# Kernel optimization log

Measured on AMD Instinct MI355X. Metric: run time of the kernel, lower is better.

The kernel has to match this reference:

```python
import jax, jax.numpy as jnp
import numpy as np

N = 100000   # nodes
E = 640000   # edges
DIN = 128
DOUT = 128
BN_EPS = 1e-5


def setup_inputs() -> dict:
    key = jax.random.key(0)
    k = jax.random.split(key, 6)
    x = jax.random.normal(k[0], (N, DIN), dtype=jnp.float32)
    edge_index = jax.random.randint(k[1], (2, E), 0, N, dtype=jnp.int64)
    # MLP params: Linear(DIN,DOUT) -> BatchNorm1d(DOUT) -> ReLU -> Linear(DOUT,DOUT)
    s1 = 1.0 / np.sqrt(DIN)
    s2 = 1.0 / np.sqrt(DOUT)
    W1 = jax.random.uniform(k[2], (DIN, DOUT), jnp.float32, -s1, s1)
    b1 = jax.random.uniform(k[3], (DOUT,), jnp.float32, -s1, s1)
    gamma = jnp.ones((DOUT,), jnp.float32)
    beta = jnp.zeros((DOUT,), jnp.float32)
    W2 = jax.random.uniform(k[4], (DOUT, DOUT), jnp.float32, -s2, s2)
    b2 = jax.random.uniform(k[5], (DOUT,), jnp.float32, -s2, s2)
    eps = jnp.zeros((), jnp.float32)  # train_eps=True, init 0.0
    return {"x": x, "edge_index": edge_index, "W1": W1, "b1": b1,
            "gamma": gamma, "beta": beta, "W2": W2, "b2": b2, "eps": eps}


def reference(x, edge_index, W1, b1, gamma, beta, W2, b2, eps):
    src = edge_index[0]
    dst = edge_index[1]
    # GIN sum aggregation: gather source features, scatter-add to target nodes
    agg = jax.ops.segment_sum(x[src], dst, num_segments=N)  # [N, DIN]
    h = agg + (1.0 + eps) * x  # eps-weighted residual combine
    # MLP: Linear -> BatchNorm1d (training stats, biased var) -> ReLU -> Linear
    h = h @ W1 + b1  # [N, DOUT]
    mu = jnp.mean(h, axis=0)
    var = jnp.mean((h - mu) ** 2, axis=0)
    h = (h - mu) * jax.lax.rsqrt(var + BN_EPS) * gamma + beta
    h = jnp.maximum(h, 0.0)
    return h @ W2 + b2
```

## Files before the change

### kernel.cpp

```cpp
#include <hip/hip_runtime.h>

#define N_NODES 100000
#define DIM     128
#define NEDGE   640000
#define BN_EPS  1e-5f
#define NB_SCAN 98

#define PB_X    6250
#define PB_W    64
#define PB_CNT  2500

#define NBUCKET 64
#define T_TILES 4
#define GGRID   1563

typedef __bf16 bf16x8 __attribute__((ext_vector_type(8)));
typedef float  f32x4  __attribute__((ext_vector_type(4)));
typedef unsigned short u16x8 __attribute__((ext_vector_type(8)));

__device__ __forceinline__ unsigned short f2b(float f) {
    unsigned u = __builtin_bit_cast(unsigned, f);
    u += 0x7fffu + ((u >> 16) & 1u);
    return (unsigned short)(u >> 16);
}
__device__ __forceinline__ float b2f(unsigned short b) {
    return __builtin_bit_cast(float, ((unsigned)b) << 16);
}

__global__ __launch_bounds__(256) void k_prep(const float* __restrict__ x,
                                              const float* __restrict__ W1,
                                              const float* __restrict__ W2,
                                              const int* __restrict__ ei,
                                              unsigned short* __restrict__ xb,
                                              unsigned short* __restrict__ Wt1,
                                              unsigned short* __restrict__ Wt2,
                                              int* __restrict__ rowptr,
                                              unsigned short* __restrict__ rank) {
    const int b = blockIdx.x;
    const int t = threadIdx.x;
    if (b < PB_X) {
        size_t base = ((size_t)b * 256 + t) * 8;
        float4 v0 = *(const float4*)(x + base);
        float4 v1 = *(const float4*)(x + base + 4);
        u16x8 o;
        o[0] = f2b(v0.x); o[1] = f2b(v0.y); o[2] = f2b(v0.z); o[3] = f2b(v0.w);
        o[4] = f2b(v1.x); o[5] = f2b(v1.y); o[6] = f2b(v1.z); o[7] = f2b(v1.w);
        *(u16x8*)(xb + base) = o;
    } else if (b < PB_X + PB_W) {
        int idx = (b - PB_X) * 256 + t;
        int k = idx >> 7, n = idx & 127;
        Wt1[n * 128 + k] = f2b(W1[idx]);
    } else if (b < PB_X + 2 * PB_W) {
        int idx = (b - PB_X - PB_W) * 256 + t;
        int k = idx >> 7, n = idx & 127;
        Wt2[n * 128 + k] = f2b(W2[idx]);
    } else {
        int e = (b - PB_X - 2 * PB_W) * 256 + t;
        if (e < NEDGE) {
            int r = atomicAdd(&rowptr[ei[NEDGE + e]], 1);
            rank[e] = (unsigned short)r;
        }
    }
}

__global__ __launch_bounds__(256) void k_scan1(int* __restrict__ rowptr,
                                               int* __restrict__ bsum) {
    __shared__ int tsum[256];
    const int t = threadIdx.x;
    const int base = blockIdx.x * 1024 + t * 4;
    int v[4];
    #pragma unroll
    for (int j = 0; j < 4; ++j)
        v[j] = (base + j < N_NODES) ? rowptr[base + j] : 0;
    int s = v[0] + v[1] + v[2] + v[3];
    tsum[t] = s;
    __syncthreads();
    #pragma unroll
    for (int off = 1; off < 256; off <<= 1) {
        int a = tsum[t];
        int b = (t >= off) ? tsum[t - off] : 0;
        __syncthreads();
        tsum[t] = a + b;
        __syncthreads();
    }
    int run = tsum[t] - s;
    #pragma unroll
    for (int j = 0; j < 4; ++j) {
        int nv = run;
        run += v[j];
        if (base + j < N_NODES) rowptr[base + j] = nv;
    }
    if (t == 255) bsum[blockIdx.x] = tsum[255];
}

__global__ __launch_bounds__(256) void k_scan_add(int* __restrict__ rowptr,
                                                  const int* __restrict__ bsum) {
    __shared__ int sh[128];
    const int t = threadIdx.x;
    if (t < 128) sh[t] = (t < NB_SCAN) ? bsum[t] : 0;
    __syncthreads();
    #pragma unroll
    for (int off = 1; off < 128; off <<= 1) {
        int a = 0, b = 0;
        if (t < 128) { a = sh[t]; b = (t >= off) ? sh[t - off] : 0; }
        __syncthreads();
        if (t < 128) sh[t] = a + b;
        __syncthreads();
    }
    const int add = (blockIdx.x > 0) ? sh[blockIdx.x - 1] : 0;
    const int base = blockIdx.x * 1024 + t * 4;
    #pragma unroll
    for (int j = 0; j < 4; ++j) {
        if (base + j < N_NODES) rowptr[base + j] += add;
    }
    if (blockIdx.x == 0 && t == 0) rowptr[N_NODES] = NEDGE;
}

__global__ __launch_bounds__(256) void k_fill(const int* __restrict__ ei,
                                              const int* __restrict__ rowptr,
                                              const unsigned short* __restrict__ rank,
                                              int* __restrict__ srcidx) {
    int e = blockIdx.x * 256 + threadIdx.x;
    if (e < NEDGE) {
        int dst = ei[NEDGE + e];
        srcidx[rowptr[dst] + (int)rank[e]] = ei[e];
    }
}

__global__ __launch_bounds__(256) void k_agg1(const unsigned short* __restrict__ xb,
                                              const int* __restrict__ rowptr,
                                              const int* __restrict__ srcidx,
                                              const float* __restrict__ epsp,
                                              const unsigned short* __restrict__ Wt,
                                              const float* __restrict__ b1,
                                              unsigned short* __restrict__ hB,
                                              float* __restrict__ buckets) {
    __shared__ float sl[256];
    __shared__ __align__(16) unsigned short At[2][16 * 136];
    __shared__ __align__(16) unsigned short stage[4][512];
    const int t = threadIdx.x;
    const int w = t >> 6;
    const int lane = t & 63;
    const int n15 = lane & 15;
    const int quad = lane >> 4;
    const int c8 = n15 * 8;

    int4 Bfr[2][4];
    const unsigned short* wp = Wt + (w * 32 + n15) * 128 + quad * 8;
    #pragma unroll
    for (int c = 0; c < 2; ++c)
        #pragma unroll
        for (int ks = 0; ks < 4; ++ks)
            Bfr[c][ks] = *(const int4*)(wp + c * 16 * 128 + ks * 32);
    float bias[2] = { b1[w * 32 + n15], b1[w * 32 + 16 + n15] };
    const float scale = 1.0f + epsp[0];

    const int tile0 = blockIdx.x * T_TILES;
    float s[2] = {0.f, 0.f}, q[2] = {0.f, 0.f};
    unsigned short* st = stage[w];

    #pragma unroll
    for (int i = 0; i < T_TILES; ++i) {
        const int row0 = (tile0 + i) * 16;
        const bool valid = row0 < N_NODES;
        unsigned short* al = At[i & 1];
        if (valid) {
            const int node = row0 + w * 4 + quad;
            float acc[8];
            {
                u16x8 v = *(const u16x8*)(xb + (size_t)node * 128 + c8);
                #pragma unroll
                for (int j = 0; j < 8; ++j) acc[j] = scale * b2f(v[j]);
            }
            const int beg = rowptr[node];
            const int end = rowptr[node + 1];
            for (int p = beg; p < end; p += 2) {
                int s0 = srcidx[p];
                u16x8 v0 = *(const u16x8*)(xb + (size_t)s0 * 128 + c8);
                const bool h1 = (p + 1) < end;
                u16x8 v1;
                if (h1) {
                    int s1 = srcidx[p + 1];
                    v1 = *(const u16x8*)(xb + (size_t)s1 * 128 + c8);
                }
                #pragma unroll
                for (int j = 0; j < 8; ++j) acc[j] += b2f(v0[j]);
                if (h1) {
                    #pragma unroll
                    for (int j = 0; j < 8; ++j) acc[j] += b2f(v1[j]);
                }
            }
            u16x8 o;
            #pragma unroll
            for (int j = 0; j < 8; ++j) o[j] = f2b(acc[j]);
            *(u16x8*)(al + (w * 4 + quad) * 136 + c8) = o;
        }
        __syncthreads();
        if (valid) {
            f32x4 accm[2] = {};
            #pragma unroll
            for (int ks = 0; ks < 4; ++ks) {
                int4 araw = *(const int4*)(al + n15 * 136 + ks * 32 + quad * 8);
                bf16x8 af = __builtin_bit_cast(bf16x8, araw);
                #pragma unroll
                for (int c = 0; c < 2; ++c)
                    accm[c] = __builtin_amdgcn_mfma_f32_16x16x32_bf16(
                        af, __builtin_bit_cast(bf16x8, Bfr[c][ks]), accm[c], 0, 0, 0);
            }
            #pragma unroll
            for (int c = 0; c < 2; ++c)
                #pragma unroll
                for (int r = 0; r < 4; ++r) {
                    float v = accm[c][r] + bias[c];
                    s[c] += v; q[c] += v * v;
                    st[(quad * 4 + r) * 32 + c * 16 + n15] = f2b(v);
                }
            int so = lane * 8;
            int r = so >> 5, cc = so & 31;
            *(int4*)(hB + (size_t)(row0 + r) * 128 + w * 32 + cc) = *(const int4*)(st + so);
        }
    }

    #pragma unroll
    for (int c = 0; c < 2; ++c) {
        s[c] += __shfl_down(s[c], 32); q[c] += __shfl_down(q[c], 32);
        s[c] += __shfl_down(s[c], 16); q[c] += __shfl_down(q[c], 16);
    }
    if (quad == 0) {
        #pragma unroll
        for (int c = 0; c < 2; ++c) {
            sl[w * 32 + c * 16 + n15] = s[c];
            sl[128 + w * 32 + c * 16 + n15] = q[c];
        }
    }
    __syncthreads();
    atomicAdd(&buckets[(blockIdx.x & (NBUCKET - 1)) * 256 + t], sl[t]);
}

__global__ void k_finalize(const float* __restrict__ gamma,
                           const float* __restrict__ beta,
                           const float* __restrict__ buckets,
                           float* __restrict__ aff) {
    int c = threadIdx.x;
    if (c < DIM) {
        float s = 0.f, q = 0.f;
        #pragma unroll 8
        for (int b = 0; b < NBUCKET; ++b) {
            s += buckets[b * 256 + c];
            q += buckets[b * 256 + 128 + c];
        }
        float mu  = s * (1.0f / N_NODES);
        float var = q * (1.0f / N_NODES) - mu * mu;
        float a = gamma[c] * rsqrtf(var + BN_EPS);
        aff[c] = a;
        aff[DIM + c] = beta[c] - mu * a;
    }
}

__global__ __launch_bounds__(256) void k_gemm2(const unsigned short* __restrict__ hb,
                                               const unsigned short* __restrict__ Wt2,
                                               const float* __restrict__ aff,
                                               const float* __restrict__ b2,
                                               float* __restrict__ out) {
    __shared__ __align__(16) unsigned short Asb[2][16 * 136];
    __shared__ __align__(16) float stage[4][512];
    const int t = threadIdx.x;
    const int w = t >> 6;
    const int lane = t & 63;
    const int n15 = lane & 15;
    const int quad = lane >> 4;
    const int kb = w * 32 + quad * 8;

    int4 Bfr[2][4];
    const unsigned short* wp = Wt2 + (w * 32 + n15) * 128 + quad * 8;
    #pragma unroll
    for (int c = 0; c < 2; ++c)
        #pragma unroll
        for (int ks = 0; ks < 4; ++ks)
            Bfr[c][ks] = *(const int4*)(wp + c * 16 * 128 + ks * 32);

    float akr[8], bkr[8];
    *(float4*)(akr)     = *(const float4*)(aff + kb);
    *(float4*)(akr + 4) = *(const float4*)(aff + kb + 4);
    *(float4*)(bkr)     = *(const float4*)(aff + 128 + kb);
    *(float4*)(bkr + 4) = *(const float4*)(aff + 128 + kb + 4);
    float bias[2] = { b2[w * 32 + n15], b2[w * 32 + 16 + n15] };

    const int tile0 = blockIdx.x * T_TILES;
    int4 gr;
    {
        int r0 = tile0 * 16;
        if (r0 < N_NODES)
            gr = *(const int4*)(hb + (size_t)(r0 + n15) * 128 + kb);
    }
    float* st = stage[w];

    #pragma unroll
    for (int i = 0; i < T_TILES; ++i) {
        const int row0 = (tile0 + i) * 16;
        const bool valid = row0 < N_NODES;
        unsigned short* al = Asb[i & 1];
        if (valid) {
            u16x8 ar = __builtin_bit_cast(u16x8, gr);
            u16x8 pr;
            #pragma unroll
            for (int j = 0; j < 8; ++j)
                pr[j] = f2b(fmaxf(fmaf(b2f(ar[j]), akr[j], bkr[j]), 0.f));
            *(int4*)(al + n15 * 136 + kb) = __builtin_bit_cast(int4, pr);
        }
        if (i + 1 < T_TILES) {
            int rn = (tile0 + i + 1) * 16;
            if (rn < N_NODES)
                gr = *(const int4*)(hb + (size_t)(rn + n15) * 128 + kb);
        }
        __syncthreads();
        if (valid) {
            f32x4 acc[2] = {};
            #pragma unroll
            for (int ks = 0; ks < 4; ++ks) {
                int4 araw = *(const int4*)(al + n15 * 136 + ks * 32 + quad * 8);
                bf16x8 af = __builtin_bit_cast(bf16x8, araw);
                #pragma unroll
                for (int c = 0; c < 2; ++c)
                    acc[c] = __builtin_amdgcn_mfma_f32_16x16x32_bf16(
                        af, __builtin_bit_cast(bf16x8, Bfr[c][ks]), acc[c], 0, 0, 0);
            }
            #pragma unroll
            for (int c = 0; c < 2; ++c)
                #pragma unroll
                for (int r = 0; r < 4; ++r)
                    st[(quad * 4 + r) * 32 + c * 16 + n15] = acc[c][r] + bias[c];
            #pragma unroll
            for (int p = 0; p < 2; ++p) {
                int fo = p * 256 + lane * 4;
                int r = fo >> 5, cc = fo & 31;
                *(float4*)(out + (size_t)(row0 + r) * 128 + w * 32 + cc) =
                    *(const float4*)(st + fo);
            }
        }
    }
}

extern "C" void kernel_launch(void* const* d_in, const int* in_sizes, int n_in,
                              void* d_out, int out_size, void* d_ws, size_t ws_size,
                              hipStream_t stream) {
    const float* x     = (const float*)d_in[0];
    const int*   ei    = (const int*)d_in[1];
    const float* W1    = (const float*)d_in[2];
    const float* b1    = (const float*)d_in[3];
    const float* gamma = (const float*)d_in[4];
    const float* beta  = (const float*)d_in[5];
    const float* W2    = (const float*)d_in[6];
    const float* b2    = (const float*)d_in[7];
    const float* eps   = (const float*)d_in[8];
    float* out = (float*)d_out;

    float* buckets      = (float*)d_ws;
    int* rowptr         = (int*)(buckets + NBUCKET * 256);
    float* aff          = (float*)(rowptr + N_NODES + 4);
    unsigned short* hB  = (unsigned short*)(aff + 256);
    unsigned short* xb  = hB + (size_t)N_NODES * DIM;
    unsigned short* Wt1 = xb + (size_t)N_NODES * DIM;
    unsigned short* Wt2 = Wt1 + 16384;
    int* srcidx         = (int*)(Wt2 + 16384);
    int* bsum           = srcidx + NEDGE;
    unsigned short* rank = hB;

    hipMemsetAsync(buckets, 0,
                   NBUCKET * 256 * sizeof(float) + (N_NODES + 4) * sizeof(int), stream);

    k_prep<<<PB_X + 2 * PB_W + PB_CNT, 256, 0, stream>>>(x, W1, W2, ei, xb, Wt1, Wt2,
                                                         rowptr, rank);
    k_scan1<<<NB_SCAN, 256, 0, stream>>>(rowptr, bsum);
    k_scan_add<<<NB_SCAN, 256, 0, stream>>>(rowptr, bsum);
    k_fill<<<(NEDGE + 255) / 256, 256, 0, stream>>>(ei, rowptr, rank, srcidx);
    k_agg1<<<GGRID, 256, 0, stream>>>(xb, rowptr, srcidx, eps, Wt1, b1, hB, buckets);
    k_finalize<<<1, 128, 0, stream>>>(gamma, beta, buckets, aff);
    k_gemm2<<<GGRID, 256, 0, stream>>>(hB, Wt2, aff, b2, out);
}
```

Baseline: 240.9 us.

## Process one 16-node tile per aggregation block with 4-way unrolled neighbor gather

The aggregation+GEMM1 kernel now handles a single 16-row tile per block (6250 blocks instead of 1563 blocks looping over 4 tiles). The neighbor gather issues four independent row loads per iteration instead of two. The per-block BN statistics go straight to global atomics from quad-0 lanes, which drops the shared reduction and its barrier. The prep kernel also moves the edge-counting atomics to the first blocks so they start earlier. The aim is more memory-level parallelism and less in-block serialization, at the cost of reloading the W1 fragments in 4x as many blocks and issuing more atomics to the buckets.

After: 229.8 us. -4.6%, faster.

```diff
diff --git a/kernel.cpp b/kernel.cpp
--- a/kernel.cpp
+++ b/kernel.cpp
@@ -6,13 +6,14 @@
 #define BN_EPS  1e-5f
 #define NB_SCAN 98
 
+#define PB_CNT  2500
 #define PB_X    6250
 #define PB_W    64
-#define PB_CNT  2500
 
 #define NBUCKET 64
 #define T_TILES 4
 #define GGRID   1563
+#define AGRID   6250
 
 typedef __bf16 bf16x8 __attribute__((ext_vector_type(8)));
 typedef float  f32x4  __attribute__((ext_vector_type(4)));
@@ -38,28 +39,26 @@
                                               unsigned short* __restrict__ rank) {
     const int b = blockIdx.x;
     const int t = threadIdx.x;
-    if (b < PB_X) {
-        size_t base = ((size_t)b * 256 + t) * 8;
+    if (b < PB_CNT) {
+        int e = b * 256 + t;
+        int r = atomicAdd(&rowptr[ei[NEDGE + e]], 1);
+        rank[e] = (unsigned short)r;
+    } else if (b < PB_CNT + PB_X) {
+        size_t base = ((size_t)(b - PB_CNT) * 256 + t) * 8;
         float4 v0 = *(const float4*)(x + base);
         float4 v1 = *(const float4*)(x + base + 4);
         u16x8 o;
         o[0] = f2b(v0.x); o[1] = f2b(v0.y); o[2] = f2b(v0.z); o[3] = f2b(v0.w);
         o[4] = f2b(v1.x); o[5] = f2b(v1.y); o[6] = f2b(v1.z); o[7] = f2b(v1.w);
         *(u16x8*)(xb + base) = o;
-    } else if (b < PB_X + PB_W) {
-        int idx = (b - PB_X) * 256 + t;
+    } else if (b < PB_CNT + PB_X + PB_W) {
+        int idx = (b - PB_CNT - PB_X) * 256 + t;
         int k = idx >> 7, n = idx & 127;
         Wt1[n * 128 + k] = f2b(W1[idx]);
-    } else if (b < PB_X + 2 * PB_W) {
-        int idx = (b - PB_X - PB_W) * 256 + t;
+    } else {
+        int idx = (b - PB_CNT - PB_X - PB_W) * 256 + t;
         int k = idx >> 7, n = idx & 127;
         Wt2[n * 128 + k] = f2b(W2[idx]);
-    } else {
-        int e = (b - PB_X - 2 * PB_W) * 256 + t;
-        if (e < NEDGE) {
-            int r = atomicAdd(&rowptr[ei[NEDGE + e]], 1);
-            rank[e] = (unsigned short)r;
-        }
     }
 }
 
@@ -135,8 +134,7 @@
                                               const float* __restrict__ b1,
                                               unsigned short* __restrict__ hB,
                                               float* __restrict__ buckets) {
-    __shared__ float sl[256];
-    __shared__ __align__(16) unsigned short At[2][16 * 136];
+    __shared__ __align__(16) unsigned short At[16 * 136];
     __shared__ __align__(16) unsigned short stage[4][512];
     const int t = threadIdx.x;
     const int w = t >> 6;
@@ -145,6 +143,9 @@
     const int quad = lane >> 4;
     const int c8 = n15 * 8;
 
+    const int row0 = blockIdx.x * 16;
+    const int node = row0 + w * 4 + quad;
+
     int4 Bfr[2][4];
     const unsigned short* wp = Wt + (w * 32 + n15) * 128 + quad * 8;
     #pragma unroll
@@ -155,70 +156,71 @@
     float bias[2] = { b1[w * 32 + n15], b1[w * 32 + 16 + n15] };
     const float scale = 1.0f + epsp[0];
 
-    const int tile0 = blockIdx.x * T_TILES;
+    const int beg = rowptr[node];
+    const int end = rowptr[node + 1];
+    float acc[8];
+    {
+        u16x8 v = *(const u16x8*)(xb + (size_t)node * 128 + c8);
+        #pragma unroll
+        for (int j = 0; j < 8; ++j) acc[j] = scale * b2f(v[j]);
+    }
+    for (int p = beg; p < end; p += 4) {
+        const int np = end - p;
+        int i0 = srcidx[p];
+        int i1 = (np > 1) ? srcidx[p + 1] : i0;
+        int i2 = (np > 2) ? srcidx[p + 2] : i0;
+        int i3 = (np > 3) ? srcidx[p + 3] : i0;
+        u16x8 v0 = *(const u16x8*)(xb + (size_t)i0 * 128 + c8);
+        u16x8 v1 = *(const u16x8*)(xb + (size_t)i1 * 128 + c8);
+        u16x8 v2 = *(const u16x8*)(xb + (size_t)i2 * 128 + c8);
+        u16x8 v3 = *(const u16x8*)(xb + (size_t)i3 * 128 + c8);
+        #pragma unroll
+        for (int j = 0; j < 8; ++j) acc[j] += b2f(v0[j]);
+        if (np > 1) {
+            #pragma unroll
+            for (int j = 0; j < 8; ++j) acc[j] += b2f(v1[j]);
+        }
+        if (np > 2) {
+            #pragma unroll
+            for (int j = 0; j < 8; ++j) acc[j] += b2f(v2[j]);
+        }
+        if (np > 3) {
+            #pragma unroll
+            for (int j = 0; j < 8; ++j) acc[j] += b2f(v3[j]);
+        }
+    }
+    {
+        u16x8 o;
+        #pragma unroll
+        for (int j = 0; j < 8; ++j) o[j] = f2b(acc[j]);
+        *(u16x8*)(At + (w * 4 + quad) * 136 + c8) = o;
+    }
+    __syncthreads();
+
+    f32x4 accm[2] = {};
+    #pragma unroll
+    for (int ks = 0; ks < 4; ++ks) {
+        int4 araw = *(const int4*)(At + n15 * 136 + ks * 32 + quad * 8);
+        bf16x8 af = __builtin_bit_cast(bf16x8, araw);
+        #pragma unroll
+        for (int c = 0; c < 2; ++c)
+            accm[c] = __builtin_amdgcn_mfma_f32_16x16x32_bf16(
+                af, __builtin_bit_cast(bf16x8, Bfr[c][ks]), accm[c], 0, 0, 0);
+    }
     float s[2] = {0.f, 0.f}, q[2] = {0.f, 0.f};
     unsigned short* st = stage[w];
-
-    #pragma unroll
-    for (int i = 0; i < T_TILES; ++i) {
-        const int row0 = (tile0 + i) * 16;
-        const bool valid = row0 < N_NODES;
-        unsigned short* al = At[i & 1];
-        if (valid) {
-            const int node = row0 + w * 4 + quad;
-            float acc[8];
-            {
-                u16x8 v = *(const u16x8*)(xb + (size_t)node * 128 + c8);
-                #pragma unroll
-                for (int j = 0; j < 8; ++j) acc[j] = scale * b2f(v[j]);
-            }
-            const int beg = rowptr[node];
-            const int end = rowptr[node + 1];
-            for (int p = beg; p < end; p += 2) {
-                int s0 = srcidx[p];
-                u16x8 v0 = *(const u16x8*)(xb + (size_t)s0 * 128 + c8);
-                const bool h1 = (p + 1) < end;
-                u16x8 v1;
-                if (h1) {
-                    int s1 = srcidx[p + 1];
-                    v1 = *(const u16x8*)(xb + (size_t)s1 * 128 + c8);
-                }
-                #pragma unroll
-                for (int j = 0; j < 8; ++j) acc[j] += b2f(v0[j]);
-                if (h1) {
-                    #pragma unroll
-                    for (int j = 0; j < 8; ++j) acc[j] += b2f(v1[j]);
-                }
-            }
-            u16x8 o;
-            #pragma unroll
-            for (int j = 0; j < 8; ++j) o[j] = f2b(acc[j]);
-            *(u16x8*)(al + (w * 4 + quad) * 136 + c8) = o;
-        }
-        __syncthreads();
-        if (valid) {
-            f32x4 accm[2] = {};
-            #pragma unroll
-            for (int ks = 0; ks < 4; ++ks) {
-                int4 araw = *(const int4*)(al + n15 * 136 + ks * 32 + quad * 8);
-                bf16x8 af = __builtin_bit_cast(bf16x8, araw);
-                #pragma unroll
-                for (int c = 0; c < 2; ++c)
-                    accm[c] = __builtin_amdgcn_mfma_f32_16x16x32_bf16(
-                        af, __builtin_bit_cast(bf16x8, Bfr[c][ks]), accm[c], 0, 0, 0);
-            }
-            #pragma unroll
-            for (int c = 0; c < 2; ++c)
-                #pragma unroll
-                for (int r = 0; r < 4; ++r) {
-                    float v = accm[c][r] + bias[c];
-                    s[c] += v; q[c] += v * v;
-                    st[(quad * 4 + r) * 32 + c * 16 + n15] = f2b(v);
-                }
-            int so = lane * 8;
-            int r = so >> 5, cc = so & 31;
-            *(int4*)(hB + (size_t)(row0 + r) * 128 + w * 32 + cc) = *(const int4*)(st + so);
-        }
+    #pragma unroll
+    for (int c = 0; c < 2; ++c)
+        #pragma unroll
+        for (int r = 0; r < 4; ++r) {
+            float v = accm[c][r] + bias[c];
+            s[c] += v; q[c] += v * v;
+            st[(quad * 4 + r) * 32 + c * 16 + n15] = f2b(v);
+        }
+    {
+        int so = lane * 8;
+        int r = so >> 5, cc = so & 31;
+        *(int4*)(hB + (size_t)(row0 + r) * 128 + w * 32 + cc) = *(const int4*)(st + so);
     }
 
     #pragma unroll
@@ -227,14 +229,12 @@
         s[c] += __shfl_down(s[c], 16); q[c] += __shfl_down(q[c], 16);
     }
     if (quad == 0) {
-        #pragma unroll
-        for (int c = 0; c < 2; ++c) {
-            sl[w * 32 + c * 16 + n15] = s[c];
-            sl[128 + w * 32 + c * 16 + n15] = q[c];
-        }
-    }
-    __syncthreads();
-    atomicAdd(&buckets[(blockIdx.x & (NBUCKET - 1)) * 256 + t], sl[t]);
+        float* bk = buckets + (blockIdx.x & (NBUCKET - 1)) * 256;
+        atomicAdd(&bk[w * 32 + n15], s[0]);
+        atomicAdd(&bk[w * 32 + 16 + n15], s[1]);
+        atomicAdd(&bk[128 + w * 32 + n15], q[0]);
+        atomicAdd(&bk[128 + w * 32 + 16 + n15], q[1]);
+    }
 }
 
 __global__ void k_finalize(const float* __restrict__ gamma,
@@ -369,12 +369,12 @@
     hipMemsetAsync(buckets, 0,
                    NBUCKET * 256 * sizeof(float) + (N_NODES + 4) * sizeof(int), stream);
 
-    k_prep<<<PB_X + 2 * PB_W + PB_CNT, 256, 0, stream>>>(x, W1, W2, ei, xb, Wt1, Wt2,
+    k_prep<<<PB_CNT + PB_X + 2 * PB_W, 256, 0, stream>>>(x, W1, W2, ei, xb, Wt1, Wt2,
                                                          rowptr, rank);
     k_scan1<<<NB_SCAN, 256, 0, stream>>>(rowptr, bsum);
     k_scan_add<<<NB_SCAN, 256, 0, stream>>>(rowptr, bsum);
     k_fill<<<(NEDGE + 255) / 256, 256, 0, stream>>>(ei, rowptr, rank, srcidx);
-    k_agg1<<<GGRID, 256, 0, stream>>>(xb, rowptr, srcidx, eps, Wt1, b1, hB, buckets);
+    k_agg1<<<AGRID, 256, 0, stream>>>(xb, rowptr, srcidx, eps, Wt1, b1, hB, buckets);
     k_finalize<<<1, 128, 0, stream>>>(gamma, beta, buckets, aff);
     k_gemm2<<<GGRID, 256, 0, stream>>>(hB, Wt2, aff, b2, out);
 }
```
